# Kernel tuning notes

Measured on AMD Instinct MI355X. Metric: run time of the kernel, lower is better.

Reference implementation:

```python
import jax, jax.numpy as jnp
import numpy as np

B, C, T, V, K, O = 16, 256, 128, 64, 8, 256


def conv1x1(x, w, b):
    # x: [B,C,T,V], w: [O,C], b: [O] -> [B,O,T,V]
    return jnp.einsum('bctv,oc->botv', x, w) + b[None, :, None, None]


def batchnorm(x, gamma, beta, eps=1e-5):
    # training-mode BatchNorm2d: stats over (B,T,V) per channel
    mean = x.mean(axis=(0, 2, 3), keepdims=True)
    var = x.var(axis=(0, 2, 3), keepdims=True)
    return gamma[None, :, None, None] * (x - mean) * jax.lax.rsqrt(var + eps) + beta[None, :, None, None]


def setup_inputs() -> dict:
    key = jax.random.key(0)
    ks = jax.random.split(key, 16)
    inp = {
        'x': jax.random.normal(ks[0], (B, C, T, V), jnp.float32),
        'A_param': jax.random.normal(ks[1], (1, K, 1, V, V), jnp.float32) * 0.1,
        'alpha': jax.random.normal(ks[2], (), jnp.float32) * 0.1,
        'beta': jax.random.normal(ks[3], (), jnp.float32) * 0.1,
        'w1': jax.random.normal(ks[4], (O, C), jnp.float32) * 0.02,
        'b1': jax.random.normal(ks[5], (O,), jnp.float32) * 0.02,
        'w2': jax.random.normal(ks[6], (O, C), jnp.float32) * 0.02,
        'b2': jax.random.normal(ks[7], (O,), jnp.float32) * 0.02,
        'stem_w': jax.random.normal(ks[8], (O, C), jnp.float32) * 0.02,
        'stem_b': jax.random.normal(ks[9], (O,), jnp.float32) * 0.02,
        'stem_gamma': jnp.ones((O,), jnp.float32),
        'stem_beta': jnp.zeros((O,), jnp.float32),
        'head_w': jax.random.normal(ks[10], (O, O), jnp.float32) * 0.02,
        'head_b': jax.random.normal(ks[11], (O,), jnp.float32) * 0.02,
        'head_gamma': jnp.ones((O,), jnp.float32),
        'head_beta': jnp.zeros((O,), jnp.float32),
    }
    return inp


def reference(x, A_param, alpha, beta, w1, b1, w2, b2,
              stem_w, stem_b, stem_gamma, stem_beta,
              head_w, head_b, head_gamma, head_beta):
    b_, c_, t_, v_ = x.shape
    k_ = A_param.shape[1]
    tp = x.mean(axis=2, keepdims=True)                      # [B,C,1,V]
    x1 = conv1x1(tp, w1, b1).reshape(b_, k_, -1, v_)        # [B,K,c,V]
    x2 = conv1x1(tp, w2, b2).reshape(b_, k_, -1, v_)
    ctr = jnp.tanh(x1[..., :, None] - x2[..., None, :])     # [B,K,c,V,V]
    ada = jax.nn.softmax(jnp.einsum('bkcv,bkcw->bkvw', x1, x2)[:, :, None], axis=-2)  # [B,K,1,V,V]
    A = A_param + ctr * alpha + ada * beta                  # [B,K,c,V,V]
    res = x                                                 # in_channels == out_channels -> Identity
    h = jax.nn.relu(batchnorm(conv1x1(x, stem_w, stem_b), stem_gamma, stem_beta))
    h = h.reshape(b_, k_, -1, t_, v_)                       # [B,K,c,T,V]
    h = jnp.einsum('bkctv,bkcvw->bkctw', h, A).reshape(b_, -1, t_, v_)
    return jax.nn.relu(batchnorm(conv1x1(h, head_w, head_b), head_gamma, head_beta) + res)
```

## Files before the change

kernel.cpp:

```cpp
#include <hip/hip_runtime.h>
#include <cstdint>
#include <cstddef>

#define B_ 16
#define C_ 256
#define T_ 128
#define V_ 64
#define K_ 8
#define O_ 256
#define TN 8192
#define NBT 131072
#define NSL 32

typedef unsigned short ushort_t;
typedef __attribute__((ext_vector_type(8))) short short8;
typedef __attribute__((ext_vector_type(4))) float f32x4;

#define OFF_TP     0
#define OFF_X1     262144
#define OFF_X2     524288
#define OFF_STATS  786432
#define OFF_SSC    819200
#define OFF_HSC    819712
#define OFF_ADA    820224
#define OFF_Z      1344512
#define OFF_H2     34867200

__device__ inline ushort_t f2bf(float f) {
    unsigned u = __builtin_bit_cast(unsigned, f);
    unsigned r = (u + 0x7FFFu + ((u >> 16) & 1u)) >> 16;
    return (ushort_t)r;
}
__device__ inline unsigned pack2(float a, float b) {
    return (unsigned)f2bf(a) | ((unsigned)f2bf(b) << 16);
}
__device__ inline float bf2f_lo(unsigned u) { return __builtin_bit_cast(float, u << 16); }
__device__ inline float bf2f_hi(unsigned u) { return __builtin_bit_cast(float, u & 0xFFFF0000u); }
__device__ inline void gload_lds16(const void* g, void* l) {
    __builtin_amdgcn_global_load_lds((const __attribute__((address_space(1))) unsigned int*)g,
                                     (__attribute__((address_space(3))) unsigned int*)l, 16, 0, 0);
}

__global__ __launch_bounds__(512) void k_xpose2(const float* __restrict__ x,
                                                ushort_t* __restrict__ img,
                                                float* __restrict__ tp) {
    __shared__ float L[8 * 2048];
    int tq = blockIdx.x;
    int cg = blockIdx.y;
    int b  = blockIdx.z;
    int tid  = threadIdx.x;
    int wv   = tid >> 6;
    int lane = tid & 63;
    int t0 = tq * 32;

    float4 vreg[8];
    auto load_regs = [&](int g) {
        int c = cg * 32 + g * 8 + wv;
        const float* src = x + ((size_t)(b * C_ + c) * 128 + t0) * 64 + lane * 4;
        #pragma unroll
        for (int i = 0; i < 8; i++)
            vreg[i] = *(const float4*)(src + i * 256);
    };

    load_regs(0);
    for (int g = 0; g < 4; g++) {
        float4 s4 = {0.f, 0.f, 0.f, 0.f};
        #pragma unroll
        for (int i = 0; i < 8; i++) {
            *(float4*)&L[wv * 2048 + i * 256 + lane * 4] = vreg[i];
            s4.x += vreg[i].x; s4.y += vreg[i].y;
            s4.z += vreg[i].z; s4.w += vreg[i].w;
        }
        s4.x += __shfl_xor(s4.x, 16, 64); s4.y += __shfl_xor(s4.y, 16, 64);
        s4.z += __shfl_xor(s4.z, 16, 64); s4.w += __shfl_xor(s4.w, 16, 64);
        s4.x += __shfl_xor(s4.x, 32, 64); s4.y += __shfl_xor(s4.y, 32, 64);
        s4.z += __shfl_xor(s4.z, 32, 64); s4.w += __shfl_xor(s4.w, 32, 64);
        if (lane < 16) {
            int c = cg * 32 + g * 8 + wv;
            const float r = 1.0f / (float)T_;
            float* dst = tp + (size_t)(b * C_ + c) * V_ + lane * 4;
            atomicAdd(&dst[0], s4.x * r); atomicAdd(&dst[1], s4.y * r);
            atomicAdd(&dst[2], s4.z * r); atomicAdd(&dst[3], s4.w * r);
        }
        __syncthreads();
        if (g < 3) load_regs(g + 1);

        int v = tid & 63, tw = tid >> 6;
        size_t obase = ((size_t)(b * 128 + t0) * 8 + cg) * 2048 + g * 512 + (size_t)v * 8;
        #pragma unroll
        for (int s = 0; s < 4; s++) {
            int tl = s * 8 + tw;
            const float* Lp = &L[tl * 64 + v];
            uint4 u;
            u.x = pack2(Lp[0 * 2048], Lp[1 * 2048]);
            u.y = pack2(Lp[2 * 2048], Lp[3 * 2048]);
            u.z = pack2(Lp[4 * 2048], Lp[5 * 2048]);
            u.w = pack2(Lp[6 * 2048], Lp[7 * 2048]);
            *(uint4*)(img + obase + (size_t)tl * 16384) = u;
        }
        __syncthreads();
    }
}

__global__ __launch_bounds__(256) void k_x1x2a(const float* __restrict__ tp,
                                               const float* __restrict__ w1, const float* __restrict__ b1,
                                               const float* __restrict__ w2, const float* __restrict__ b2,
                                               float* __restrict__ x1, float* __restrict__ x2) {
    int og = blockIdx.x, cc = blockIdx.y, b = blockIdx.z;
    int o  = og * 16 + (threadIdx.x >> 4);
    int v4 = threadIdx.x & 15;
    const float4* ptp = (const float4*)(tp + (size_t)b * C_ * V_) + v4;
    float4 s1 = {0.f,0.f,0.f,0.f}, s2 = {0.f,0.f,0.f,0.f};
    int c0 = cc * 64;
    for (int c = c0; c < c0 + 64; c++) {
        float4 tv = ptp[c * 16];
        float wa = w1[o * C_ + c];
        float wb = w2[o * C_ + c];
        s1.x += tv.x * wa; s1.y += tv.y * wa; s1.z += tv.z * wa; s1.w += tv.w * wa;
        s2.x += tv.x * wb; s2.y += tv.y * wb; s2.z += tv.z * wb; s2.w += tv.w * wb;
    }
    if (cc == 0) {
        float bv1 = b1[o], bv2 = b2[o];
        s1.x += bv1; s1.y += bv1; s1.z += bv1; s1.w += bv1;
        s2.x += bv2; s2.y += bv2; s2.z += bv2; s2.w += bv2;
    }
    float* p1 = x1 + (size_t)(b * O_ + o) * V_ + v4 * 4;
    float* p2 = x2 + (size_t)(b * O_ + o) * V_ + v4 * 4;
    atomicAdd(&p1[0], s1.x); atomicAdd(&p1[1], s1.y); atomicAdd(&p1[2], s1.z); atomicAdd(&p1[3], s1.w);
    atomicAdd(&p2[0], s2.x); atomicAdd(&p2[1], s2.y); atomicAdd(&p2[2], s2.z); atomicAdd(&p2[3], s2.w);
}

__global__ __launch_bounds__(64) void k_ada(const float* __restrict__ x1,
                                            const float* __restrict__ x2,
                                            float* __restrict__ ada) {
    int bid = blockIdx.x;
    int w = bid & 63;
    int k = (bid >> 6) & 7;
    int b = bid >> 9;
    int v = threadIdx.x;
    const float* p1 = x1 + ((size_t)b * O_ + k * 32) * V_;
    const float* p2 = x2 + ((size_t)b * O_ + k * 32) * V_;
    float s = 0.f;
    #pragma unroll
    for (int c = 0; c < 32; c++) s += p1[c * V_ + v] * p2[c * V_ + w];
    float m = s;
    #pragma unroll
    for (int off = 32; off >= 1; off >>= 1) m = fmaxf(m, __shfl_xor(m, off, 64));
    float e = __expf(s - m);
    float sum = e;
    #pragma unroll
    for (int off = 32; off >= 1; off >>= 1) sum += __shfl_xor(sum, off, 64);
    ada[((size_t)(b * K_ + k) * V_ + v) * V_ + w] = e / sum;
}

__global__ __launch_bounds__(256) void k_wconv(const float* __restrict__ ws,
                                               const float* __restrict__ wh,
                                               ushort_t* __restrict__ img) {
    const float* w = blockIdx.y ? wh : ws;
    ushort_t* dst = img + (size_t)blockIdx.y * 65536;
    int flat = blockIdx.x * 256 + threadIdx.x;
    #pragma unroll
    for (int g2 = 0; g2 < 2; g2++) {
        int gi = flat * 2 + g2;
        int cc = gi >> 10;
        int q  = (gi >> 8) & 3;
        int ol = gi & 255;
        int c0 = cc * 32 + q * 8;
        const float* src = w + (size_t)ol * C_ + c0;
        float4 f0 = *(const float4*)src;
        float4 f1 = *(const float4*)(src + 4);
        uint4 u;
        u.x = pack2(f0.x, f0.y); u.y = pack2(f0.z, f0.w);
        u.z = pack2(f1.x, f1.y); u.w = pack2(f1.z, f1.w);
        *(uint4*)(dst + (size_t)gi * 8) = u;
    }
}

__global__ __launch_bounds__(256) void k_gemm(const ushort_t* __restrict__ ximg,
                                              const ushort_t* __restrict__ wimg,
                                              const float* __restrict__ bias,
                                              ushort_t* __restrict__ out,
                                              float* __restrict__ psum,
                                              float* __restrict__ psumsq) {
    __shared__ __align__(16) ushort_t sh[2][2048];
    int tid = threadIdx.x;
    int nblk = blockIdx.x, b = blockIdx.z;
    int wm = tid >> 6;
    int lane = tid & 63, ln = lane & 15, q = lane >> 4;
    f32x4 acc[4][4];
    #pragma unroll
    for (int mt = 0; mt < 4; mt++)
        #pragma unroll
        for (int nt = 0; nt < 4; nt++) acc[mt][nt] = (f32x4){0.f, 0.f, 0.f, 0.f};
    const ushort_t* xbase = ximg + ((size_t)(b * 128 + nblk) * 8) * 2048;
    gload_lds16(xbase + wm * 512 + lane * 8, &sh[0][wm * 512]);
    __syncthreads();
    for (int cc = 0; cc < 8; cc++) {
        int cur = cc & 1;
        if (cc < 7)
            gload_lds16(xbase + (size_t)(cc + 1) * 2048 + wm * 512 + lane * 8,
                        &sh[cur ^ 1][wm * 512]);
        short8 a[4], bb[4];
        const ushort_t* wc = wimg + (size_t)cc * 8192 + q * 2048;
        #pragma unroll
        for (int mt = 0; mt < 4; mt++)
            a[mt] = *(const short8*)(wc + (wm * 64 + mt * 16 + ln) * 8);
        #pragma unroll
        for (int nt = 0; nt < 4; nt++)
            bb[nt] = *(const short8*)&sh[cur][q * 512 + (nt * 16 + ln) * 8];
        #pragma unroll
        for (int mt = 0; mt < 4; mt++)
            #pragma unroll
            for (int nt = 0; nt < 4; nt++)
                acc[mt][nt] = __builtin_amdgcn_mfma_f32_16x16x32_bf16(a[mt], bb[nt], acc[mt][nt], 0, 0, 0);
        __syncthreads();
    }
    int n_base = nblk * 64;
    int slice = (nblk ^ (b << 3)) & (NSL - 1);
    #pragma unroll
    for (int mt = 0; mt < 4; mt++) {
        int o0 = wm * 64 + mt * 16 + q * 4;
        #pragma unroll
        for (int r = 0; r < 4; r++) {
            float bv = bias[o0 + r];
            float v0 = acc[mt][0][r] + bv, v1 = acc[mt][1][r] + bv;
            float v2 = acc[mt][2][r] + bv, v3 = acc[mt][3][r] + bv;
            ushort_t* orow = out + ((size_t)(b * O_ + o0 + r)) * TN + n_base + ln;
            orow[0] = f2bf(v0); orow[16] = f2bf(v1); orow[32] = f2bf(v2); orow[48] = f2bf(v3);
            float s  = v0 + v1 + v2 + v3;
            float sq = v0 * v0 + v1 * v1 + v2 * v2 + v3 * v3;
            #pragma unroll
            for (int off = 1; off <= 8; off <<= 1) {
                s  += __shfl_xor(s,  off, 64);
                sq += __shfl_xor(sq, off, 64);
            }
            if (ln == 0) {
                atomicAdd(&psum[slice * 256 + o0 + r],   s);
                atomicAdd(&psumsq[slice * 256 + o0 + r], sq);
            }
        }
    }
}

__global__ void k_finalize(const float* __restrict__ psum, const float* __restrict__ psumsq,
                           const float* __restrict__ gamma, const float* __restrict__ betap,
                           float* __restrict__ scale, float* __restrict__ shift) {
    int o = threadIdx.x;
    float s = 0.f, sq = 0.f;
    #pragma unroll
    for (int sl = 0; sl < NSL; sl++) {
        s  += psum[sl * 256 + o];
        sq += psumsq[sl * 256 + o];
    }
    float mean = s  * (1.0f / (float)NBT);
    float var  = sq * (1.0f / (float)NBT) - mean * mean;
    float sc = gamma[o] * rsqrtf(var + 1e-5f);
    scale[o] = sc;
    shift[o] = betap[o] - mean * sc;
}

__global__ __launch_bounds__(256) void k_einsum_mfma(const ushort_t* __restrict__ z,
                                                     const float* __restrict__ x1,
                                                     const float* __restrict__ x2,
                                                     const float* __restrict__ ada,
                                                     const float* __restrict__ A_param,
                                                     const float* __restrict__ alphap,
                                                     const float* __restrict__ betap,
                                                     const float* __restrict__ ssum,
                                                     const float* __restrict__ ssq,
                                                     const float* __restrict__ sgamma,
                                                     const float* __restrict__ sbeta,
                                                     ushort_t* __restrict__ h2img) {
    __shared__ float ComT[64][65];
    __shared__ float x1s[8][64], x2s[8][64];
    __shared__ __align__(16) ushort_t stg[16 * 520];
    __shared__ float scv8[8], shv8[8];
    int tid = threadIdx.x;
    int bid = blockIdx.x;
    int q  = bid & 3;
    int k  = (bid >> 2) & 7;
    int b  = bid >> 5;
    int wm = tid >> 6;
    int lane = tid & 63, ln = lane & 15, qq = lane >> 4;
    float alpha = alphap[0], beta = betap[0];

    if (tid < 64) {
        int ch = tid >> 3, part = tid & 7;
        int o = k * 32 + q * 8 + ch;
        float s = 0.f, sq2 = 0.f;
        #pragma unroll
        for (int i = 0; i < 4; i++) {
            int sl = part * 4 + i;
            s   += ssum[sl * 256 + o];
            sq2 += ssq[sl * 256 + o];
        }
        s += __shfl_down(s, 4, 64);  sq2 += __shfl_down(sq2, 4, 64);
        s += __shfl_down(s, 2, 64);  sq2 += __shfl_down(sq2, 2, 64);
        s += __shfl_down(s, 1, 64);  sq2 += __shfl_down(sq2, 1, 64);
        if (part == 0) {
            float mean = s * (1.0f / (float)NBT);
            float var  = sq2 * (1.0f / (float)NBT) - mean * mean;
            float sc = sgamma[o] * rsqrtf(var + 1e-5f);
            scv8[ch] = sc;
            shv8[ch] = sbeta[o] - mean * sc;
        }
    }

    const float* Apk = A_param + (size_t)k * 4096;
    const float* adk = ada + (size_t)(b * K_ + k) * 4096;
    #pragma unroll
    for (int i = 0; i < 4; i++) {
        int e4 = tid + i * 256;
        int v = e4 >> 4, w4 = (e4 & 15) * 4;
        float4 ap = *(const float4*)(Apk + (size_t)e4 * 4);
        float4 ad = *(const float4*)(adk + (size_t)e4 * 4);
        ComT[w4 + 0][v] = ap.x + beta * ad.x;
        ComT[w4 + 1][v] = ap.y + beta * ad.y;
        ComT[w4 + 2][v] = ap.z + beta * ad.z;
        ComT[w4 + 3][v] = ap.w + beta * ad.w;
    }
    #pragma unroll
    for (int i = 0; i < 2; i++) {
        int e = tid + i * 256;
        int cl = e >> 6, v = e & 63;
        int o1 = k * 32 + q * 8 + cl;
        x1s[cl][v] = x1[((size_t)b * O_ + o1) * V_ + v];
        x2s[cl][v] = x2[((size_t)b * O_ + o1) * V_ + v];
    }
    __syncthreads();

    short8 bfrag[2][2][4];
    #pragma unroll
    for (int half = 0; half < 2; half++) {
        int cl = wm + half * 4;
        #pragma unroll
        for (int kk = 0; kk < 2; kk++) {
            float x1v[8];
            #pragma unroll
            for (int j = 0; j < 8; j++) x1v[j] = x1s[cl][kk * 32 + qq * 8 + j];
            #pragma unroll
            for (int nt = 0; nt < 4; nt++) {
                int w = nt * 16 + ln;
                float x2v = x2s[cl][w];
                float av[8];
                #pragma unroll
                for (int j = 0; j < 8; j++) {
                    int v = kk * 32 + qq * 8 + j;
                    float d = x1v[j] - x2v;
                    float ax = fabsf(d);
                    float e2 = __expf(-2.f * ax);
                    float th = copysignf((1.f - e2) / (1.f + e2), d);
                    av[j] = ComT[w][v] + alpha * th;
                }
                uint4 bp;
                bp.x = pack2(av[0], av[1]); bp.y = pack2(av[2], av[3]);
                bp.z = pack2(av[4], av[5]); bp.w = pack2(av[6], av[7]);
                bfrag[half][kk][nt] = __builtin_bit_cast(short8, bp);
            }
        }
    }

    int o1a = k * 32 + q * 8 + wm;
    float scv[2] = {scv8[wm], scv8[wm + 4]};
    float shv[2] = {shv8[wm], shv8[wm + 4]};
    const ushort_t* zr[2] = {z + ((size_t)b * O_ + o1a) * TN,
                             z + ((size_t)b * O_ + o1a + 4) * TN};
    size_t obase = ((size_t)(b * 128) * 8 + k) * 2048 + q * 512;

    uint4 zc[2][2];
    #pragma unroll
    for (int half = 0; half < 2; half++)
        #pragma unroll
        for (int kk = 0; kk < 2; kk++)
            zc[half][kk] = *(const uint4*)(zr[half] + (0 * 16 + ln) * 64 + kk * 32 + qq * 8);

    for (int mt = 0; mt < 8; mt++) {
        uint4 zn[2][2];
        if (mt < 7) {
            #pragma unroll
            for (int half = 0; half < 2; half++)
                #pragma unroll
                for (int kk = 0; kk < 2; kk++)
                    zn[half][kk] = *(const uint4*)(zr[half] + ((mt + 1) * 16 + ln) * 64 + kk * 32 + qq * 8);
        }
        f32x4 acc[2][4];
        #pragma unroll
        for (int half = 0; half < 2; half++)
            #pragma unroll
            for (int nt = 0; nt < 4; nt++) acc[half][nt] = (f32x4){0.f, 0.f, 0.f, 0.f};
        #pragma unroll
        for (int half = 0; half < 2; half++) {
            float s = scv[half], h = shv[half];
            #pragma unroll
            for (int kk = 0; kk < 2; kk++) {
                uint4 zv = zc[half][kk];
                float f0 = bf2f_lo(zv.x), f1 = bf2f_hi(zv.x);
                float f2 = bf2f_lo(zv.y), f3 = bf2f_hi(zv.y);
                float f4 = bf2f_lo(zv.z), f5 = bf2f_hi(zv.z);
                float f6 = bf2f_lo(zv.w), f7 = bf2f_hi(zv.w);
                uint4 hp;
                hp.x = pack2(fmaxf(f0 * s + h, 0.f), fmaxf(f1 * s + h, 0.f));
                hp.y = pack2(fmaxf(f2 * s + h, 0.f), fmaxf(f3 * s + h, 0.f));
                hp.z = pack2(fmaxf(f4 * s + h, 0.f), fmaxf(f5 * s + h, 0.f));
                hp.w = pack2(fmaxf(f6 * s + h, 0.f), fmaxf(f7 * s + h, 0.f));
                short8 hf = __builtin_bit_cast(short8, hp);
                #pragma unroll
                for (int nt = 0; nt < 4; nt++)
                    acc[half][nt] = __builtin_amdgcn_mfma_f32_16x16x32_bf16(hf, bfrag[half][kk][nt], acc[half][nt], 0, 0, 0);
            }
        }
        #pragma unroll
        for (int half = 0; half < 2; half++) {
            int cl = wm + half * 4;
            #pragma unroll
            for (int nt = 0; nt < 4; nt++)
                #pragma unroll
                for (int r = 0; r < 4; r++)
                    stg[(qq * 4 + r) * 520 + (nt * 16 + ln) * 8 + cl] = f2bf(acc[half][nt][r]);
        }
        __syncthreads();
        #pragma unroll
        for (int ii = 0; ii < 4; ii++) {
            int u = tid + ii * 256;
            int tl = u >> 6, off = u & 63;
            ((uint4*)(h2img + obase + (size_t)(mt * 16 + tl) * 16384))[off] =
                ((const uint4*)stg)[tl * 65 + off];
        }
        __syncthreads();
        if (mt < 7) {
            #pragma unroll
            for (int half = 0; half < 2; half++)
                #pragma unroll
                for (int kk = 0; kk < 2; kk++)
                    zc[half][kk] = zn[half][kk];
        }
    }
}

__global__ __launch_bounds__(256) void k_final(const ushort_t* __restrict__ ub,
                                               const float* __restrict__ x,
                                               const float* __restrict__ scale,
                                               const float* __restrict__ shift,
                                               float* __restrict__ out) {
    size_t i4 = (size_t)blockIdx.x * 256 + threadIdx.x;
    int o = (int)((i4 >> 11) & 255);
    uint2 uv = ((const uint2*)ub)[i4];
    float4 xv = ((const float4*)x)[i4];
    float sc = scale[o], sh = shift[o];
    float4 r;
    r.x = fmaxf(bf2f_lo(uv.x) * sc + sh + xv.x, 0.f);
    r.y = fmaxf(bf2f_hi(uv.x) * sc + sh + xv.y, 0.f);
    r.z = fmaxf(bf2f_lo(uv.y) * sc + sh + xv.z, 0.f);
    r.w = fmaxf(bf2f_hi(uv.y) * sc + sh + xv.w, 0.f);
    ((float4*)out)[i4] = r;
}

extern "C" void kernel_launch(void* const* d_in, const int* in_sizes, int n_in,
                              void* d_out, int out_size, void* d_ws, size_t ws_size,
                              hipStream_t stream) {
    const float* x          = (const float*)d_in[0];
    const float* A_param    = (const float*)d_in[1];
    const float* alphap     = (const float*)d_in[2];
    const float* betap      = (const float*)d_in[3];
    const float* w1         = (const float*)d_in[4];
    const float* b1         = (const float*)d_in[5];
    const float* w2         = (const float*)d_in[6];
    const float* b2         = (const float*)d_in[7];
    const float* stem_w     = (const float*)d_in[8];
    const float* stem_b     = (const float*)d_in[9];
    const float* stem_gamma = (const float*)d_in[10];
    const float* stem_beta  = (const float*)d_in[11];
    const float* head_w     = (const float*)d_in[12];
    const float* head_b     = (const float*)d_in[13];
    const float* head_gamma = (const float*)d_in[14];
    const float* head_beta  = (const float*)d_in[15];

    float* W      = (float*)d_ws;
    float* tp     = W + OFF_TP;
    float* x1b    = W + OFF_X1;
    float* x2b    = W + OFF_X2;
    float* ssum   = W + OFF_STATS;
    float* ssq    = W + OFF_STATS + NSL * 256;
    float* hsum   = W + OFF_STATS + NSL * 512;
    float* hsq    = W + OFF_STATS + NSL * 768;
    float* hscale = W + OFF_HSC;
    float* hshift = W + OFF_HSC + 256;
    float* adab   = W + OFF_ADA;
    float* uout   = (float*)d_out;

    ushort_t* xTimg  = (ushort_t*)d_out;
    ushort_t* wsimg  = (ushort_t*)(W + OFF_TP);
    ushort_t* zb16   = (ushort_t*)(W + OFF_Z);
    ushort_t* ub16   = zb16;
    ushort_t* h2img  = (ushort_t*)(W + OFF_H2);

    hipMemsetAsync(W, 0, (size_t)(OFF_STATS + NSL * 1024) * sizeof(float), stream);

    k_xpose2<<<dim3(4, 8, 16), 512, 0, stream>>>(x, xTimg, tp);
    k_x1x2a<<<dim3(16, 4, 16), 256, 0, stream>>>(tp, w1, b1, w2, b2, x1b, x2b);
    k_ada<<<8192, 64, 0, stream>>>(x1b, x2b, adab);
    k_wconv<<<dim3(16, 2), 256, 0, stream>>>(stem_w, head_w, wsimg);

    k_gemm<<<dim3(128, 1, 16), 256, 0, stream>>>(xTimg, wsimg, stem_b, zb16, ssum, ssq);

    k_einsum_mfma<<<512, 256, 0, stream>>>(zb16, x1b, x2b, adab, A_param, alphap, betap,
                                           ssum, ssq, stem_gamma, stem_beta, h2img);

    k_gemm<<<dim3(128, 1, 16), 256, 0, stream>>>(h2img, wsimg + 65536, head_b, ub16, hsum, hsq);
    k_finalize<<<1, 256, 0, stream>>>(hsum, hsq, head_gamma, head_beta, hscale, hshift);
    k_final<<<32768, 256, 0, stream>>>(ub16, x, hscale, hshift, uout);
}
```

Before: 482.9 us.

## Fuse small kernels into neighbours and stage GEMM output through LDS

Removes three small launches: the weight bf16 conversion runs as an extra z-slice of the transpose kernel, the softmax adjacency is computed inside the einsum kernel from x1/x2 staged in shared memory, and BN finalize is computed per block inside the final elementwise kernel. The GEMM epilogue now writes bf16 results through an LDS staging tile so global stores become 16-byte coalesced rows instead of scattered 2-byte stores. This cuts launch overhead and global traffic for the ada tensor, at the cost of redundant ada computation per einsum block, redundant stat reduction in every final block, and extra LDS use and syncs in the GEMM.

```diff
diff --git a/kernel.cpp b/kernel.cpp
--- a/kernel.cpp
+++ b/kernel.cpp
@@ -20,9 +20,7 @@
 #define OFF_X1     262144
 #define OFF_X2     524288
 #define OFF_STATS  786432
-#define OFF_SSC    819200
-#define OFF_HSC    819712
-#define OFF_ADA    820224
+#define OFF_WIMG   820224
 #define OFF_Z      1344512
 #define OFF_H2     34867200
 
@@ -43,12 +41,36 @@
 
 __global__ __launch_bounds__(512) void k_xpose2(const float* __restrict__ x,
                                                 ushort_t* __restrict__ img,
-                                                float* __restrict__ tp) {
+                                                float* __restrict__ tp,
+                                                const float* __restrict__ stem_w,
+                                                const float* __restrict__ head_w,
+                                                ushort_t* __restrict__ wimg) {
     __shared__ float L[8 * 2048];
     int tq = blockIdx.x;
     int cg = blockIdx.y;
     int b  = blockIdx.z;
     int tid  = threadIdx.x;
+
+    if (b == 16) {
+        int flat = cg * 4 + tq;
+        int gi2 = flat * 512 + tid;
+        int m  = gi2 >> 13;
+        int gi = gi2 & 8191;
+        const float* w = m ? head_w : stem_w;
+        int cc = gi >> 10;
+        int q  = (gi >> 8) & 3;
+        int ol = gi & 255;
+        int c0 = cc * 32 + q * 8;
+        const float* src = w + (size_t)ol * C_ + c0;
+        float4 f0 = *(const float4*)src;
+        float4 f1 = *(const float4*)(src + 4);
+        uint4 u;
+        u.x = pack2(f0.x, f0.y); u.y = pack2(f0.z, f0.w);
+        u.z = pack2(f1.x, f1.y); u.w = pack2(f1.z, f1.w);
+        *(uint4*)(wimg + (size_t)m * 65536 + (size_t)gi * 8) = u;
+        return;
+    }
+
     int wv   = tid >> 6;
     int lane = tid & 63;
     int t0 = tq * 32;
@@ -130,52 +152,6 @@
     atomicAdd(&p2[0], s2.x); atomicAdd(&p2[1], s2.y); atomicAdd(&p2[2], s2.z); atomicAdd(&p2[3], s2.w);
 }
 
-__global__ __launch_bounds__(64) void k_ada(const float* __restrict__ x1,
-                                            const float* __restrict__ x2,
-                                            float* __restrict__ ada) {
-    int bid = blockIdx.x;
-    int w = bid & 63;
-    int k = (bid >> 6) & 7;
-    int b = bid >> 9;
-    int v = threadIdx.x;
-    const float* p1 = x1 + ((size_t)b * O_ + k * 32) * V_;
-    const float* p2 = x2 + ((size_t)b * O_ + k * 32) * V_;
-    float s = 0.f;
-    #pragma unroll
-    for (int c = 0; c < 32; c++) s += p1[c * V_ + v] * p2[c * V_ + w];
-    float m = s;
-    #pragma unroll
-    for (int off = 32; off >= 1; off >>= 1) m = fmaxf(m, __shfl_xor(m, off, 64));
-    float e = __expf(s - m);
-    float sum = e;
-    #pragma unroll
-    for (int off = 32; off >= 1; off >>= 1) sum += __shfl_xor(sum, off, 64);
-    ada[((size_t)(b * K_ + k) * V_ + v) * V_ + w] = e / sum;
-}
-
-__global__ __launch_bounds__(256) void k_wconv(const float* __restrict__ ws,
-                                               const float* __restrict__ wh,
-                                               ushort_t* __restrict__ img) {
-    const float* w = blockIdx.y ? wh : ws;
-    ushort_t* dst = img + (size_t)blockIdx.y * 65536;
-    int flat = blockIdx.x * 256 + threadIdx.x;
-    #pragma unroll
-    for (int g2 = 0; g2 < 2; g2++) {
-        int gi = flat * 2 + g2;
-        int cc = gi >> 10;
-        int q  = (gi >> 8) & 3;
-        int ol = gi & 255;
-        int c0 = cc * 32 + q * 8;
-        const float* src = w + (size_t)ol * C_ + c0;
-        float4 f0 = *(const float4*)src;
-        float4 f1 = *(const float4*)(src + 4);
-        uint4 u;
-        u.x = pack2(f0.x, f0.y); u.y = pack2(f0.z, f0.w);
-        u.z = pack2(f1.x, f1.y); u.w = pack2(f1.z, f1.w);
-        *(uint4*)(dst + (size_t)gi * 8) = u;
-    }
-}
-
 __global__ __launch_bounds__(256) void k_gemm(const ushort_t* __restrict__ ximg,
                                               const ushort_t* __restrict__ wimg,
                                               const float* __restrict__ bias,
@@ -183,6 +159,7 @@
                                               float* __restrict__ psum,
                                               float* __restrict__ psumsq) {
     __shared__ __align__(16) ushort_t sh[2][2048];
+    __shared__ __align__(16) ushort_t stg[64 * 72];
     int tid = threadIdx.x;
     int nblk = blockIdx.x, b = blockIdx.z;
     int wm = tid >> 6;
@@ -219,14 +196,17 @@
     int slice = (nblk ^ (b << 3)) & (NSL - 1);
     #pragma unroll
     for (int mt = 0; mt < 4; mt++) {
-        int o0 = wm * 64 + mt * 16 + q * 4;
         #pragma unroll
         for (int r = 0; r < 4; r++) {
+            int o0 = wm * 64 + mt * 16 + q * 4;
             float bv = bias[o0 + r];
             float v0 = acc[mt][0][r] + bv, v1 = acc[mt][1][r] + bv;
             float v2 = acc[mt][2][r] + bv, v3 = acc[mt][3][r] + bv;
-            ushort_t* orow = out + ((size_t)(b * O_ + o0 + r)) * TN + n_base + ln;
-            orow[0] = f2bf(v0); orow[16] = f2bf(v1); orow[32] = f2bf(v2); orow[48] = f2bf(v3);
+            int row = wm * 16 + q * 4 + r;
+            stg[row * 72 +  0 + ln] = f2bf(v0);
+            stg[row * 72 + 16 + ln] = f2bf(v1);
+            stg[row * 72 + 32 + ln] = f2bf(v2);
+            stg[row * 72 + 48 + ln] = f2bf(v3);
             float s  = v0 + v1 + v2 + v3;
             float sq = v0 * v0 + v1 * v1 + v2 * v2 + v3 * v3;
             #pragma unroll
@@ -239,30 +219,22 @@
                 atomicAdd(&psumsq[slice * 256 + o0 + r], sq);
             }
         }
-    }
-}
-
-__global__ void k_finalize(const float* __restrict__ psum, const float* __restrict__ psumsq,
-                           const float* __restrict__ gamma, const float* __restrict__ betap,
-                           float* __restrict__ scale, float* __restrict__ shift) {
-    int o = threadIdx.x;
-    float s = 0.f, sq = 0.f;
-    #pragma unroll
-    for (int sl = 0; sl < NSL; sl++) {
-        s  += psum[sl * 256 + o];
-        sq += psumsq[sl * 256 + o];
-    }
-    float mean = s  * (1.0f / (float)NBT);
-    float var  = sq * (1.0f / (float)NBT) - mean * mean;
-    float sc = gamma[o] * rsqrtf(var + 1e-5f);
-    scale[o] = sc;
-    shift[o] = betap[o] - mean * sc;
+        __syncthreads();
+        #pragma unroll
+        for (int ii = 0; ii < 2; ii++) {
+            int unit = tid + ii * 256;
+            int row = unit >> 3, c8 = (unit & 7) * 8;
+            int o = (row >> 4) * 64 + mt * 16 + (row & 15);
+            *(uint4*)(out + (size_t)(b * O_ + o) * TN + n_base + c8) =
+                *(const uint4*)&stg[row * 72 + c8];
+        }
+        __syncthreads();
+    }
 }
 
 __global__ __launch_bounds__(256) void k_einsum_mfma(const ushort_t* __restrict__ z,
                                                      const float* __restrict__ x1,
                                                      const float* __restrict__ x2,
-                                                     const float* __restrict__ ada,
                                                      const float* __restrict__ A_param,
                                                      const float* __restrict__ alphap,
                                                      const float* __restrict__ betap,
@@ -272,7 +244,8 @@
                                                      const float* __restrict__ sbeta,
                                                      ushort_t* __restrict__ h2img) {
     __shared__ float ComT[64][65];
-    __shared__ float x1s[8][64], x2s[8][64];
+    __shared__ float x1k[32][64], x2k[32][64];
+    __shared__ float adaS[64][65];
     __shared__ __align__(16) ushort_t stg[16 * 520];
     __shared__ float scv8[8], shv8[8];
     int tid = threadIdx.x;
@@ -306,26 +279,52 @@
         }
     }
 
+    #pragma unroll
+    for (int i = 0; i < 8; i++) {
+        int e = tid + i * 256;
+        int c = e >> 6, v = e & 63;
+        x1k[c][v] = x1[((size_t)b * O_ + k * 32 + c) * V_ + v];
+        x2k[c][v] = x2[((size_t)b * O_ + k * 32 + c) * V_ + v];
+    }
+    __syncthreads();
+
+    {
+        int w = tid >> 2, g = tid & 3;
+        float sv[16];
+        #pragma unroll
+        for (int j = 0; j < 16; j++) sv[j] = 0.f;
+        #pragma unroll
+        for (int c = 0; c < 32; c++) {
+            float x2v = x2k[c][w];
+            #pragma unroll
+            for (int j = 0; j < 16; j++) sv[j] += x1k[c][g * 16 + j] * x2v;
+        }
+        float mx = sv[0];
+        #pragma unroll
+        for (int j = 1; j < 16; j++) mx = fmaxf(mx, sv[j]);
+        mx = fmaxf(mx, __shfl_xor(mx, 1, 64));
+        mx = fmaxf(mx, __shfl_xor(mx, 2, 64));
+        float esum = 0.f;
+        #pragma unroll
+        for (int j = 0; j < 16; j++) { sv[j] = __expf(sv[j] - mx); esum += sv[j]; }
+        esum += __shfl_xor(esum, 1, 64);
+        esum += __shfl_xor(esum, 2, 64);
+        float rinv = 1.0f / esum;
+        #pragma unroll
+        for (int j = 0; j < 16; j++) adaS[g * 16 + j][w] = sv[j] * rinv;
+    }
+    __syncthreads();
+
     const float* Apk = A_param + (size_t)k * 4096;
-    const float* adk = ada + (size_t)(b * K_ + k) * 4096;
     #pragma unroll
     for (int i = 0; i < 4; i++) {
         int e4 = tid + i * 256;
         int v = e4 >> 4, w4 = (e4 & 15) * 4;
         float4 ap = *(const float4*)(Apk + (size_t)e4 * 4);
-        float4 ad = *(const float4*)(adk + (size_t)e4 * 4);
-        ComT[w4 + 0][v] = ap.x + beta * ad.x;
-        ComT[w4 + 1][v] = ap.y + beta * ad.y;
-        ComT[w4 + 2][v] = ap.z + beta * ad.z;
-        ComT[w4 + 3][v] = ap.w + beta * ad.w;
-    }
-    #pragma unroll
-    for (int i = 0; i < 2; i++) {
-        int e = tid + i * 256;
-        int cl = e >> 6, v = e & 63;
-        int o1 = k * 32 + q * 8 + cl;
-        x1s[cl][v] = x1[((size_t)b * O_ + o1) * V_ + v];
-        x2s[cl][v] = x2[((size_t)b * O_ + o1) * V_ + v];
+        ComT[w4 + 0][v] = ap.x + beta * adaS[v][w4 + 0];
+        ComT[w4 + 1][v] = ap.y + beta * adaS[v][w4 + 1];
+        ComT[w4 + 2][v] = ap.z + beta * adaS[v][w4 + 2];
+        ComT[w4 + 3][v] = ap.w + beta * adaS[v][w4 + 3];
     }
     __syncthreads();
 
@@ -337,11 +336,11 @@
         for (int kk = 0; kk < 2; kk++) {
             float x1v[8];
             #pragma unroll
-            for (int j = 0; j < 8; j++) x1v[j] = x1s[cl][kk * 32 + qq * 8 + j];
+            for (int j = 0; j < 8; j++) x1v[j] = x1k[q * 8 + cl][kk * 32 + qq * 8 + j];
             #pragma unroll
             for (int nt = 0; nt < 4; nt++) {
                 int w = nt * 16 + ln;
-                float x2v = x2s[cl][w];
+                float x2v = x2k[q * 8 + cl][w];
                 float av[8];
                 #pragma unroll
                 for (int j = 0; j < 8; j++) {
@@ -439,14 +438,36 @@
 
 __global__ __launch_bounds__(256) void k_final(const ushort_t* __restrict__ ub,
                                                const float* __restrict__ x,
-                                               const float* __restrict__ scale,
-                                               const float* __restrict__ shift,
+                                               const float* __restrict__ psum,
+                                               const float* __restrict__ psumsq,
+                                               const float* __restrict__ gamma,
+                                               const float* __restrict__ betap,
                                                float* __restrict__ out) {
-    size_t i4 = (size_t)blockIdx.x * 256 + threadIdx.x;
-    int o = (int)((i4 >> 11) & 255);
+    __shared__ float scsh[2];
+    int tid = threadIdx.x;
+    int o = (blockIdx.x >> 3) & 255;
+    if (tid < 64) {
+        int sl = tid & 31;
+        float s  = psum[sl * 256 + o];
+        float sq = psumsq[sl * 256 + o];
+        #pragma unroll
+        for (int off = 1; off <= 16; off <<= 1) {
+            s  += __shfl_xor(s,  off, 64);
+            sq += __shfl_xor(sq, off, 64);
+        }
+        if (tid == 0) {
+            float mean = s  * (1.0f / (float)NBT);
+            float var  = sq * (1.0f / (float)NBT) - mean * mean;
+            float sc = gamma[o] * rsqrtf(var + 1e-5f);
+            scsh[0] = sc;
+            scsh[1] = betap[o] - mean * sc;
+        }
+    }
+    __syncthreads();
+    float sc = scsh[0], sh = scsh[1];
+    size_t i4 = (size_t)blockIdx.x * 256 + tid;
     uint2 uv = ((const uint2*)ub)[i4];
     float4 xv = ((const float4*)x)[i4];
-    float sc = scale[o], sh = shift[o];
     float4 r;
     r.x = fmaxf(bf2f_lo(uv.x) * sc + sh + xv.x, 0.f);
     r.y = fmaxf(bf2f_hi(uv.x) * sc + sh + xv.y, 0.f);
@@ -483,30 +504,24 @@
     float* ssq    = W + OFF_STATS + NSL * 256;
     float* hsum   = W + OFF_STATS + NSL * 512;
     float* hsq    = W + OFF_STATS + NSL * 768;
-    float* hscale = W + OFF_HSC;
-    float* hshift = W + OFF_HSC + 256;
-    float* adab   = W + OFF_ADA;
     float* uout   = (float*)d_out;
 
     ushort_t* xTimg  = (ushort_t*)d_out;
-    ushort_t* wsimg  = (ushort_t*)(W + OFF_TP);
+    ushort_t* wsimg  = (ushort_t*)(W + OFF_WIMG);
     ushort_t* zb16   = (ushort_t*)(W + OFF_Z);
     ushort_t* ub16   = zb16;
     ushort_t* h2img  = (ushort_t*)(W + OFF_H2);
 
     hipMemsetAsync(W, 0, (size_t)(OFF_STATS + NSL * 1024) * sizeof(float), stream);
 
-    k_xpose2<<<dim3(4, 8, 16), 512, 0, stream>>>(x, xTimg, tp);
+    k_xpose2<<<dim3(4, 8, 17), 512, 0, stream>>>(x, xTimg, tp, stem_w, head_w, wsimg);
     k_x1x2a<<<dim3(16, 4, 16), 256, 0, stream>>>(tp, w1, b1, w2, b2, x1b, x2b);
-    k_ada<<<8192, 64, 0, stream>>>(x1b, x2b, adab);
-    k_wconv<<<dim3(16, 2), 256, 0, stream>>>(stem_w, head_w, wsimg);
 
     k_gemm<<<dim3(128, 1, 16), 256, 0, stream>>>(xTimg, wsimg, stem_b, zb16, ssum, ssq);
 
-    k_einsum_mfma<<<512, 256, 0, stream>>>(zb16, x1b, x2b, adab, A_param, alphap, betap,
+    k_einsum_mfma<<<512, 256, 0, stream>>>(zb16, x1b, x2b, A_param, alphap, betap,
                                            ssum, ssq, stem_gamma, stem_beta, h2img);
 
     k_gemm<<<dim3(128, 1, 16), 256, 0, stream>>>(h2img, wsimg + 65536, head_b, ub16, hsum, hsq);
-    k_finalize<<<1, 256, 0, stream>>>(hsum, hsq, head_gamma, head_beta, hscale, hshift);
-    k_final<<<32768, 256, 0, stream>>>(ub16, x, hscale, hshift, uout);
-}
+    k_final<<<32768, 256, 0, stream>>>(ub16, x, hsum, hsq, head_gamma, head_beta, uout);
+}
```

New measurement: 475.8 us. No clear change (-1.5%).
